# Performance work log

Measured on AMD Instinct MI355X. Metric: run time of the kernel, lower is better.

Reference implementation:

```python
import jax, jax.numpy as jnp
import numpy as np

N = 100000   # nodes
E = 1200000  # edges
IN = 128     # input feature dim
H = 64       # hidden_channels
OUT = 112    # output classes
L = 7        # num_layers
MSG_EPS = 1e-7


def _ln(x, g, b):
    mu = x.mean(-1, keepdims=True)
    v = ((x - mu) ** 2).mean(-1, keepdims=True)
    return (x - mu) / jnp.sqrt(v + 1e-5) * g + b


def _genconv(x, src, dst, t, scale, W1, b1, g1, bb1, W2, b2):
    # message: relu(x_j) + eps  (no edge attrs)
    m = jax.nn.relu(x[src]) + MSG_EPS                     # [E, H]
    z = t * m
    # numerically stable per-dst softmax over incoming edges (per channel)
    zmax = jax.lax.stop_gradient(jax.ops.segment_max(z, dst, num_segments=N))
    e = jnp.exp(z - zmax[dst])
    denom = jax.ops.segment_sum(e, dst, num_segments=N)
    agg = jax.ops.segment_sum(m * e, dst, num_segments=N) / jnp.where(denom > 0, denom, 1.0)
    # MsgNorm: x + scale * ||x|| * normalize(agg)
    msg = agg / jnp.maximum(jnp.linalg.norm(agg, axis=-1, keepdims=True), 1e-12)
    h = x + scale * msg * jnp.linalg.norm(x, axis=-1, keepdims=True)
    # GENConv MLP: Linear(H,2H) -> LayerNorm -> ReLU -> Linear(2H,H)
    u = jax.nn.relu(_ln(h @ W1 + b1, g1, bb1))
    return u @ W2 + b2


def setup_inputs() -> dict:
    key = jax.random.key(0)
    ks = jax.random.split(key, 6)
    s = 0.02
    return dict(
        x=jax.random.normal(ks[0], (N, IN), jnp.float32),
        edge_index=jax.random.randint(ks[1], (2, E), 0, N, dtype=jnp.int32),
        enc_W=jax.random.normal(ks[2], (IN, H), jnp.float32) * s,
        enc_b=jnp.zeros((H,), jnp.float32),
        t=jnp.ones((L,), jnp.float32),
        msg_scale=jnp.ones((L,), jnp.float32),
        W1=jax.random.normal(ks[3], (L, H, 2 * H), jnp.float32) * s,
        b1=jnp.zeros((L, 2 * H), jnp.float32),
        ln1_g=jnp.ones((L, 2 * H), jnp.float32),
        ln1_b=jnp.zeros((L, 2 * H), jnp.float32),
        W2=jax.random.normal(ks[4], (L, 2 * H, H), jnp.float32) * s,
        b2=jnp.zeros((L, H), jnp.float32),
        nrm_g=jnp.ones((L, H), jnp.float32),
        nrm_b=jnp.zeros((L, H), jnp.float32),
        lin_W=jax.random.normal(ks[5], (H, OUT), jnp.float32) * s,
        lin_b=jnp.zeros((OUT,), jnp.float32),
    )


def reference(x, edge_index, enc_W, enc_b, t, msg_scale, W1, b1, ln1_g, ln1_b,
              W2, b2, nrm_g, nrm_b, lin_W, lin_b):
    src, dst = edge_index[0], edge_index[1]
    h = x @ enc_W + enc_b
    # first layer: conv only (DeeperGCN forward applies layers[0].conv directly)
    h = _genconv(h, src, dst, t[0], msg_scale[0], W1[0], b1[0], ln1_g[0], ln1_b[0], W2[0], b2[0])
    # remaining layers: res+ block  x + conv(dropout(relu(norm(x))))  (dropout=identity at eval)
    for i in range(1, L):
        r = jax.nn.relu(_ln(h, nrm_g[i], nrm_b[i]))
        h = h + _genconv(r, src, dst, t[i], msg_scale[i], W1[i], b1[i], ln1_g[i], ln1_b[i], W2[i], b2[i])
    h = jax.nn.relu(_ln(h, nrm_g[0], nrm_b[0]))
    return h @ lin_W + lin_b
```

## Files before the change

### kernel.cpp

```cpp
#include <hip/hip_runtime.h>

#define N_NODES 100000
#define N_EDGES 1200000
#define DIM_IN 128
#define DIM_H 64
#define DIM_H2 128
#define DIM_OUT 112
#define N_LAYERS 7

#define W1P_SZ 4608
#define W2P_SZ 4352
#define WEP_SZ 4352
#define WFP_SZ 4032

typedef __attribute__((ext_vector_type(8))) short bf16x8;
typedef __attribute__((ext_vector_type(4))) float f32x4;

__device__ __forceinline__ float wsum(float v) {
#pragma unroll
  for (int m = 1; m < 64; m <<= 1) v += __shfl_xor(v, m, 64);
  return v;
}

__device__ __forceinline__ unsigned bf16rne(float f) {
  unsigned u = __float_as_uint(f);
  return (u + 0x7fffu + ((u >> 16) & 1u)) >> 16;
}
__device__ __forceinline__ unsigned pack2bf(float lo, float hi) {
  return bf16rne(lo) | (bf16rne(hi) << 16);
}
__device__ __forceinline__ float bflo(unsigned p) { return __uint_as_float(p << 16); }
__device__ __forceinline__ float bfhi(unsigned p) { return __uint_as_float(p & 0xffff0000u); }
__device__ __forceinline__ float bfu(unsigned short u) {
  return __uint_as_float(((unsigned)u) << 16);
}
__device__ __forceinline__ float exp2r(float x) { return __builtin_amdgcn_exp2f(x); }


__global__ void k_zero_i(int* __restrict__ p, int n) {
  int i = blockIdx.x * 256 + threadIdx.x;
  if (i < n) p[i] = 0;
}

__global__ void k_hist(const int* __restrict__ dst, int* __restrict__ counts,
                       int* __restrict__ rank) {
  int e = blockIdx.x * 256 + threadIdx.x;
  if (e < N_EDGES) rank[e] = atomicAdd(&counts[dst[e]], 1);
}

__global__ void k_scan1(const int* __restrict__ counts, int* __restrict__ bsums) {
  __shared__ int sd[256];
  int t = threadIdx.x;
  int i = blockIdx.x * 256 + t;
  sd[t] = (i < N_NODES) ? counts[i] : 0;
  __syncthreads();
  for (int s = 128; s > 0; s >>= 1) {
    if (t < s) sd[t] += sd[t + s];
    __syncthreads();
  }
  if (t == 0) bsums[blockIdx.x] = sd[0];
}

__global__ void k_scan2(int* __restrict__ bsums, int nb) {
  __shared__ int sd[512];
  int t = threadIdx.x;
  int v = (t < nb) ? bsums[t] : 0;
  sd[t] = v;
  __syncthreads();
  for (int o = 1; o < 512; o <<= 1) {
    int add = (t >= o) ? sd[t - o] : 0;
    __syncthreads();
    sd[t] += add;
    __syncthreads();
  }
  if (t < nb) bsums[t] = sd[t] - v;
}

__global__ void k_scan3(const int* __restrict__ counts, const int* __restrict__ bsums,
                        int* __restrict__ offs) {
  __shared__ int sd[256];
  int t = threadIdx.x;
  int i = blockIdx.x * 256 + t;
  int v = (i < N_NODES) ? counts[i] : 0;
  sd[t] = v;
  __syncthreads();
  for (int o = 1; o < 256; o <<= 1) {
    int add = (t >= o) ? sd[t - o] : 0;
    __syncthreads();
    sd[t] += add;
    __syncthreads();
  }
  int excl = sd[t] - v + bsums[blockIdx.x];
  if (i < N_NODES) offs[i] = excl;
  if (i == N_NODES - 1) offs[N_NODES] = excl + v;
}

__global__ void k_scatter(const int* __restrict__ src, const int* __restrict__ dst,
                          const int* __restrict__ rank, const int* __restrict__ offs,
                          int* __restrict__ ssrc) {
  int e = blockIdx.x * 256 + threadIdx.x;
  if (e < N_EDGES) {
    int p = offs[dst[e]] + rank[e];
    ssrc[p] = src[e];
  }
}

__global__ void k_prepack(const float* __restrict__ W1, const float* __restrict__ W2,
                          unsigned* __restrict__ W1p, unsigned* __restrict__ W2p) {
  int L = blockIdx.y;
  const float* w1 = W1 + (size_t)L * DIM_H * DIM_H2;
  const float* w2 = W2 + (size_t)L * DIM_H2 * DIM_H;
  unsigned* o1 = W1p + (size_t)L * W1P_SZ;
  unsigned* o2 = W2p + (size_t)L * W2P_SZ;
  for (int i = blockIdx.x * 256 + threadIdx.x; i < W1P_SZ; i += gridDim.x * 256) {
    int n = i / 36, kp = i - n * 36;
    o1[i] = (kp < 32) ? pack2bf(w1[(size_t)(2 * kp) * DIM_H2 + n],
                                w1[(size_t)(2 * kp + 1) * DIM_H2 + n]) : 0u;
  }
  for (int i = blockIdx.x * 256 + threadIdx.x; i < W2P_SZ; i += gridDim.x * 256) {
    int n = i / 68, kp = i - n * 68;
    o2[i] = (kp < 64) ? pack2bf(w2[(size_t)(2 * kp) * DIM_H + n],
                                w2[(size_t)(2 * kp + 1) * DIM_H + n]) : 0u;
  }
}

__global__ void k_prepack_enc(const float* __restrict__ W, unsigned* __restrict__ Wp) {
  for (int i = blockIdx.x * 256 + threadIdx.x; i < WEP_SZ; i += gridDim.x * 256) {
    int n = i / 68, kp = i - n * 68;
    Wp[i] = (kp < 64) ? pack2bf(W[(size_t)(2 * kp) * DIM_H + n],
                                W[(size_t)(2 * kp + 1) * DIM_H + n]) : 0u;
  }
}

__global__ void k_prepack_fin(const float* __restrict__ W, unsigned* __restrict__ Wp) {
  for (int i = blockIdx.x * 256 + threadIdx.x; i < WFP_SZ; i += gridDim.x * 256) {
    int n = i / 36, kp = i - n * 36;
    Wp[i] = (kp < 32) ? pack2bf(W[(size_t)(2 * kp) * DIM_OUT + n],
                                W[(size_t)(2 * kp + 1) * DIM_OUT + n]) : 0u;
  }
}


__global__ __launch_bounds__(256, 2) void k_encoder(const float* __restrict__ x,
                                                    const unsigned* __restrict__ Wp,
                                                    const float* __restrict__ bias,
                                                    unsigned short* __restrict__ hBf) {
  __shared__ __attribute__((aligned(16))) unsigned sW[WEP_SZ];
  __shared__ __attribute__((aligned(16))) unsigned sxp[32 * 68];
  int t = threadIdx.x;
  int node0 = blockIdx.x * 32;
  int w = t >> 6, lane = t & 63;
  int fr = lane & 15, fq = lane >> 4;
  const uint4* wv4 = (const uint4*)Wp;
  for (int i = t; i < WEP_SZ / 4; i += 256) *(uint4*)&sW[i * 4] = wv4[i];
  for (int i = t; i < 2048; i += 256) {
    int row = i >> 6, kp = i & 63;
    float2 xv = *(const float2*)&x[(size_t)(node0 + row) * DIM_IN + 2 * kp];
    sxp[row * 68 + kp] = pack2bf(xv.x, xv.y);
  }
  __syncthreads();
  f32x4 acc0 = {0.f, 0.f, 0.f, 0.f}, acc1 = acc0;
#pragma unroll
  for (int s = 0; s < 4; s++) {
    int kp0 = s * 16 + fq * 4;
    bf16x8 a0 = *(const bf16x8*)&sxp[fr * 68 + kp0];
    bf16x8 a1 = *(const bf16x8*)&sxp[(16 + fr) * 68 + kp0];
    bf16x8 wf = *(const bf16x8*)&sW[(w * 16 + fr) * 68 + kp0];
    acc0 = __builtin_amdgcn_mfma_f32_16x16x32_bf16(a0, wf, acc0, 0, 0, 0);
    acc1 = __builtin_amdgcn_mfma_f32_16x16x32_bf16(a1, wf, acc1, 0, 0, 0);
  }
  float bv = bias[w * 16 + fr];
#pragma unroll
  for (int r = 0; r < 4; r++) {
    hBf[(size_t)(node0 + fq * 4 + r) * DIM_H + w * 16 + fr] =
        (unsigned short)bf16rne(acc0[r] + bv);
    hBf[(size_t)(node0 + 16 + fq * 4 + r) * DIM_H + w * 16 + fr] =
        (unsigned short)bf16rne(acc1[r] + bv);
  }
}


__global__ __launch_bounds__(256) void k_edge(const unsigned* __restrict__ xin32,
                                              const int* __restrict__ ssrc,
                                              const int* __restrict__ offs,
                                              const float* __restrict__ t_arr,
                                              const float* __restrict__ sc_arr, int layer,
                                              unsigned* __restrict__ hmid32) {
  int t = threadIdx.x;
  int wave = t >> 6, lane = t & 63;
  int half = lane >> 5, cl = lane & 31;
  int v = blockIdx.x * 8 + wave * 2 + half;
  float c2 = t_arr[layer] * 1.4426950408889634f;
  float sc = sc_arr[layer];
  int beg = offs[v], end = offs[v + 1];
  unsigned cl4 = cl << 2;
  const char* xbase = (const char*)xin32;
  unsigned xp = *(const unsigned*)(xbase + (((unsigned)v << 7) + cl4));
  float xv0 = bflo(xp), xv1 = bfhi(xp);
  float D0 = 0.f, S0 = 0.f, D1 = 0.f, S1 = 0.f;
  float D2 = 0.f, S2 = 0.f, D3 = 0.f, S3 = 0.f;
  float D4 = 0.f, S4 = 0.f, D5 = 0.f, S5 = 0.f;
  float D6 = 0.f, S6 = 0.f, D7 = 0.f, S7 = 0.f;
  int e = beg;
  for (; e + 3 < end; e += 4) {
    unsigned o0 = ((unsigned)ssrc[e] << 7) + cl4;
    unsigned o1 = ((unsigned)ssrc[e + 1] << 7) + cl4;
    unsigned o2 = ((unsigned)ssrc[e + 2] << 7) + cl4;
    unsigned o3 = ((unsigned)ssrc[e + 3] << 7) + cl4;
    unsigned u0 = *(const unsigned*)(xbase + o0);
    unsigned u1 = *(const unsigned*)(xbase + o1);
    unsigned u2 = *(const unsigned*)(xbase + o2);
    unsigned u3 = *(const unsigned*)(xbase + o3);
    float a0 = fmaxf(bflo(u0), 0.f), a1 = fmaxf(bfhi(u0), 0.f);
    float b0 = fmaxf(bflo(u1), 0.f), b1 = fmaxf(bfhi(u1), 0.f);
    float g0 = fmaxf(bflo(u2), 0.f), g1 = fmaxf(bfhi(u2), 0.f);
    float h0 = fmaxf(bflo(u3), 0.f), h1 = fmaxf(bfhi(u3), 0.f);
    float ea0 = exp2r(c2 * a0), ea1 = exp2r(c2 * a1);
    float eb0 = exp2r(c2 * b0), eb1 = exp2r(c2 * b1);
    float eg0 = exp2r(c2 * g0), eg1 = exp2r(c2 * g1);
    float eh0 = exp2r(c2 * h0), eh1 = exp2r(c2 * h1);
    D0 += ea0; S0 += a0 * ea0;
    D1 += ea1; S1 += a1 * ea1;
    D2 += eb0; S2 += b0 * eb0;
    D3 += eb1; S3 += b1 * eb1;
    D4 += eg0; S4 += g0 * eg0;
    D5 += eg1; S5 += g1 * eg1;
    D6 += eh0; S6 += h0 * eh0;
    D7 += eh1; S7 += h1 * eh1;
  }
  for (; e < end; ++e) {
    unsigned o0 = ((unsigned)ssrc[e] << 7) + cl4;
    unsigned u0 = *(const unsigned*)(xbase + o0);
    float a0 = fmaxf(bflo(u0), 0.f), a1 = fmaxf(bfhi(u0), 0.f);
    float ea0 = exp2r(c2 * a0), ea1 = exp2r(c2 * a1);
    D0 += ea0; S0 += a0 * ea0;
    D1 += ea1; S1 += a1 * ea1;
  }
  float Da = (D0 + D2) + (D4 + D6), Sa = (S0 + S2) + (S4 + S6);
  float Db = (D1 + D3) + (D5 + D7), Sb = (S1 + S3) + (S5 + S7);
  int has = (end > beg);
  float agg0 = has ? (Sa / Da + 1e-7f) : 0.f;
  float agg1 = has ? (Sb / Db + 1e-7f) : 0.f;
  float na = agg0 * agg0 + agg1 * agg1;
  float nx = xv0 * xv0 + xv1 * xv1;
#pragma unroll
  for (int m = 1; m < 32; m <<= 1) {
    na += __shfl_xor(na, m, 64);
    nx += __shfl_xor(nx, m, 64);
  }
  float inv = sc * sqrtf(nx) / fmaxf(sqrtf(na), 1e-12f);
  float r0 = xv0 + inv * agg0;
  float r1 = xv1 + inv * agg1;
  hmid32[(size_t)v * 32 + cl] = pack2bf(r0, r1);
}


__global__ __launch_bounds__(256, 2) void k_mlp(const unsigned* __restrict__ xin32,
                                                float* __restrict__ h,
                                                unsigned short* __restrict__ rnext,
                                                const unsigned* __restrict__ W1p,
                                                const float* __restrict__ b1,
                                                const float* __restrict__ g1,
                                                const float* __restrict__ bb1,
                                                const unsigned* __restrict__ W2p,
                                                const float* __restrict__ b2,
                                                const float* __restrict__ gn,
                                                const float* __restrict__ bn, int residual) {
  __shared__ unsigned short scr[4][16][136];
  int t = threadIdx.x;
  int w = t >> 6, lane = t & 63;
  int wid = blockIdx.x * 4 + w;
  if (wid >= N_NODES / 16) return;
  int node0 = wid * 16;
  int fr = lane & 15, fq = lane >> 4;

  bf16x8 xa0 = *(const bf16x8*)&xin32[(size_t)(node0 + fr) * 32 + fq * 4];
  bf16x8 xa1 = *(const bf16x8*)&xin32[(size_t)(node0 + fr) * 32 + 16 + fq * 4];
  f32x4 c1[8];
#pragma unroll
  for (int nt = 0; nt < 8; nt++) {
    f32x4 a = {0.f, 0.f, 0.f, 0.f};
    bf16x8 w0 = *(const bf16x8*)&W1p[(size_t)(nt * 16 + fr) * 36 + fq * 4];
    bf16x8 w1 = *(const bf16x8*)&W1p[(size_t)(nt * 16 + fr) * 36 + 16 + fq * 4];
    a = __builtin_amdgcn_mfma_f32_16x16x32_bf16(xa0, w0, a, 0, 0, 0);
    a = __builtin_amdgcn_mfma_f32_16x16x32_bf16(xa1, w1, a, 0, 0, 0);
    c1[nt] = a;
  }
  float b1v[8], g1v[8], bb1v[8];
#pragma unroll
  for (int nt = 0; nt < 8; nt++) {
    b1v[nt] = b1[nt * 16 + fr];
    g1v[nt] = g1[nt * 16 + fr];
    bb1v[nt] = bb1[nt * 16 + fr];
  }
#pragma unroll
  for (int r = 0; r < 4; r++) {
    float s1 = 0.f, s2 = 0.f;
#pragma unroll
    for (int nt = 0; nt < 8; nt++) {
      float u = c1[nt][r] + b1v[nt];
      s1 += u;
      s2 += u * u;
    }
#pragma unroll
    for (int m = 1; m < 16; m <<= 1) {
      s1 += __shfl_xor(s1, m, 64);
      s2 += __shfl_xor(s2, m, 64);
    }
    float mu = s1 * (1.f / 128.f);
    float var = s2 * (1.f / 128.f) - mu * mu;
    float rs = rsqrtf(var + 1e-5f);
    int row = fq * 4 + r;
#pragma unroll
    for (int nt = 0; nt < 8; nt++) {
      float u = c1[nt][r] + b1v[nt];
      u = fmaxf((u - mu) * rs * g1v[nt] + bb1v[nt], 0.f);
      scr[w][row][nt * 16 + fr] = (unsigned short)bf16rne(u);
    }
  }
  bf16x8 ua[4];
#pragma unroll
  for (int s = 0; s < 4; s++) ua[s] = *(const bf16x8*)&scr[w][fr][s * 32 + fq * 8];
  f32x4 c2[4];
#pragma unroll
  for (int nt = 0; nt < 4; nt++) {
    f32x4 a = {0.f, 0.f, 0.f, 0.f};
#pragma unroll
    for (int s = 0; s < 4; s++) {
      bf16x8 wf = *(const bf16x8*)&W2p[(size_t)(nt * 16 + fr) * 68 + s * 16 + fq * 4];
      a = __builtin_amdgcn_mfma_f32_16x16x32_bf16(ua[s], wf, a, 0, 0, 0);
    }
    c2[nt] = a;
  }
  float b2v[4], gv[4], bv[4];
#pragma unroll
  for (int nt = 0; nt < 4; nt++) {
    b2v[nt] = b2[nt * 16 + fr];
    gv[nt] = gn[nt * 16 + fr];
    bv[nt] = bn[nt * 16 + fr];
  }
#pragma unroll
  for (int r = 0; r < 4; r++) {
    int row = fq * 4 + r;
    size_t base = (size_t)(node0 + row) * DIM_H;
    float o0, o1, o2, o3, s1, s2;
    o0 = c2[0][r] + b2v[0];
    o1 = c2[1][r] + b2v[1];
    o2 = c2[2][r] + b2v[2];
    o3 = c2[3][r] + b2v[3];
    if (residual) {
      o0 += h[base + 0 * 16 + fr];
      o1 += h[base + 1 * 16 + fr];
      o2 += h[base + 2 * 16 + fr];
      o3 += h[base + 3 * 16 + fr];
    }
    s1 = (o0 + o1) + (o2 + o3);
    s2 = (o0 * o0 + o1 * o1) + (o2 * o2 + o3 * o3);
#pragma unroll
    for (int m = 1; m < 16; m <<= 1) {
      s1 += __shfl_xor(s1, m, 64);
      s2 += __shfl_xor(s2, m, 64);
    }
    float mu = s1 * (1.f / 64.f);
    float var = s2 * (1.f / 64.f) - mu * mu;
    float rs = rsqrtf(var + 1e-5f);
    h[base + 0 * 16 + fr] = o0;
    h[base + 1 * 16 + fr] = o1;
    h[base + 2 * 16 + fr] = o2;
    h[base + 3 * 16 + fr] = o3;
    rnext[base + 0 * 16 + fr] = (unsigned short)bf16rne(fmaxf((o0 - mu) * rs * gv[0] + bv[0], 0.f));
    rnext[base + 1 * 16 + fr] = (unsigned short)bf16rne(fmaxf((o1 - mu) * rs * gv[1] + bv[1], 0.f));
    rnext[base + 2 * 16 + fr] = (unsigned short)bf16rne(fmaxf((o2 - mu) * rs * gv[2] + bv[2], 0.f));
    rnext[base + 3 * 16 + fr] = (unsigned short)bf16rne(fmaxf((o3 - mu) * rs * gv[3] + bv[3], 0.f));
  }
}


__global__ __launch_bounds__(256, 2) void k_final(const unsigned* __restrict__ rB32,
                                                  const unsigned* __restrict__ Wp,
                                                  const float* __restrict__ bias,
                                                  float* __restrict__ out) {
  int t = threadIdx.x;
  int w = t >> 6, lane = t & 63;
  int wid = blockIdx.x * 4 + w;
  if (wid >= N_NODES / 16) return;
  int node0 = wid * 16;
  int fr = lane & 15, fq = lane >> 4;
  bf16x8 xa0 = *(const bf16x8*)&rB32[(size_t)(node0 + fr) * 32 + fq * 4];
  bf16x8 xa1 = *(const bf16x8*)&rB32[(size_t)(node0 + fr) * 32 + 16 + fq * 4];
#pragma unroll
  for (int nt = 0; nt < 7; nt++) {
    f32x4 a = {0.f, 0.f, 0.f, 0.f};
    bf16x8 w0 = *(const bf16x8*)&Wp[(size_t)(nt * 16 + fr) * 36 + fq * 4];
    bf16x8 w1 = *(const bf16x8*)&Wp[(size_t)(nt * 16 + fr) * 36 + 16 + fq * 4];
    a = __builtin_amdgcn_mfma_f32_16x16x32_bf16(xa0, w0, a, 0, 0, 0);
    a = __builtin_amdgcn_mfma_f32_16x16x32_bf16(xa1, w1, a, 0, 0, 0);
    float bv = bias[nt * 16 + fr];
#pragma unroll
    for (int r = 0; r < 4; r++)
      out[(size_t)(node0 + fq * 4 + r) * DIM_OUT + nt * 16 + fr] = a[r] + bv;
  }
}


extern "C" void kernel_launch(void* const* d_in, const int* in_sizes, int n_in,
                              void* d_out, int out_size, void* d_ws, size_t ws_size,
                              hipStream_t stream) {
  const float* x = (const float*)d_in[0];
  const int* ei = (const int*)d_in[1];
  const float* encW = (const float*)d_in[2];
  const float* encb = (const float*)d_in[3];
  const float* t_arr = (const float*)d_in[4];
  const float* sc_arr = (const float*)d_in[5];
  const float* W1 = (const float*)d_in[6];
  const float* b1 = (const float*)d_in[7];
  const float* g1 = (const float*)d_in[8];
  const float* bb1 = (const float*)d_in[9];
  const float* W2 = (const float*)d_in[10];
  const float* b2 = (const float*)d_in[11];
  const float* ng = (const float*)d_in[12];
  const float* nbias = (const float*)d_in[13];
  const float* linW = (const float*)d_in[14];
  const float* linb = (const float*)d_in[15];

  float* hA = (float*)d_ws;
  unsigned short* mCbf = (unsigned short*)(hA + (size_t)N_NODES * DIM_H);
  unsigned short* rBf = mCbf + (size_t)N_NODES * DIM_H;
  unsigned short* hBf = rBf + (size_t)N_NODES * DIM_H;
  int* ssrc = (int*)(hBf + (size_t)N_NODES * DIM_H);
  int* rank = ssrc + N_EDGES;
  int* offs = rank + N_EDGES;
  int* counts = offs + (N_NODES + 1);
  int* bsums = counts + N_NODES;
  unsigned* W1p = (unsigned*)(((uintptr_t)(bsums + 512) + 15) & ~(uintptr_t)15);
  unsigned* W2p = W1p + (size_t)N_LAYERS * W1P_SZ;
  unsigned* Wep = W2p + (size_t)N_LAYERS * W2P_SZ;
  unsigned* Wfp = Wep + WEP_SZ;

  const int* srcI = ei;
  const int* dstI = ei + N_EDGES;

  const int nbScan = (N_NODES + 255) / 256;
  const int nbEdge = (N_EDGES + 255) / 256;
  const int nbWave = (N_NODES / 16 + 3) / 4;

  k_zero_i<<<nbScan, 256, 0, stream>>>(counts, N_NODES);
  k_hist<<<nbEdge, 256, 0, stream>>>(dstI, counts, rank);
  k_prepack<<<dim3(3, N_LAYERS), 256, 0, stream>>>(W1, W2, W1p, W2p);
  k_prepack_enc<<<3, 256, 0, stream>>>(encW, Wep);
  k_prepack_fin<<<3, 256, 0, stream>>>(linW, Wfp);
  k_scan1<<<nbScan, 256, 0, stream>>>(counts, bsums);
  k_scan2<<<1, 512, 0, stream>>>(bsums, nbScan);
  k_scan3<<<nbScan, 256, 0, stream>>>(counts, bsums, offs);
  k_scatter<<<nbEdge, 256, 0, stream>>>(srcI, dstI, rank, offs, ssrc);

  k_encoder<<<N_NODES / 32, 256, 0, stream>>>(x, Wep, encb, hBf);

  for (int i = 0; i < N_LAYERS; i++) {
    int nx = (i + 1 < N_LAYERS) ? (i + 1) : 0;
    const unsigned* gin32 = (const unsigned*)((i == 0) ? hBf : rBf);
    k_edge<<<N_NODES / 8, 256, 0, stream>>>(gin32, ssrc, offs, t_arr, sc_arr, i,
                                            (unsigned*)mCbf);
    k_mlp<<<nbWave, 256, 0, stream>>>(
        (const unsigned*)mCbf, hA, rBf, W1p + (size_t)i * W1P_SZ, b1 + i * DIM_H2,
        g1 + i * DIM_H2, bb1 + i * DIM_H2, W2p + (size_t)i * W2P_SZ, b2 + i * DIM_H,
        ng + nx * DIM_H, nbias + nx * DIM_H, (i > 0) ? 1 : 0);
  }

  k_final<<<nbWave, 256, 0, stream>>>((const unsigned*)rBf, Wfp, linb, (float*)d_out);
}
```

Measured before the change: 585.6 us.

## Partition histogram atomics, unroll edge gather by 8, skip ReLU after first layer

The degree histogram now uses 8 partitioned count arrays, chosen by block index, to cut atomic contention on hot destination counters. The scan kernels sum the partitions and write per-partition prefix offsets, which the scatter uses to place edges. The edge aggregation kernel unrolls the gather loop to 8 edges so more loads are in flight. It is also templated to drop the ReLU for layers after the first, whose inputs are already ReLU outputs. The costs are an 8x larger count array to zero and scan, and higher register pressure in the edge kernel.

Result: faster. 555.8 us (-5.1%).

```diff
diff --git a/kernel.cpp b/kernel.cpp
--- a/kernel.cpp
+++ b/kernel.cpp
@@ -42,17 +42,23 @@
   if (i < n) p[i] = 0;
 }
 
-__global__ void k_hist(const int* __restrict__ dst, int* __restrict__ counts,
+__global__ void k_hist(const int* __restrict__ dst, int* __restrict__ counts8,
                        int* __restrict__ rank) {
   int e = blockIdx.x * 256 + threadIdx.x;
-  if (e < N_EDGES) rank[e] = atomicAdd(&counts[dst[e]], 1);
-}
-
-__global__ void k_scan1(const int* __restrict__ counts, int* __restrict__ bsums) {
+  int p = blockIdx.x & 7;
+  if (e < N_EDGES) rank[e] = atomicAdd(&counts8[(size_t)p * N_NODES + dst[e]], 1);
+}
+
+__global__ void k_scan1(const int* __restrict__ counts8, int* __restrict__ bsums) {
   __shared__ int sd[256];
   int t = threadIdx.x;
   int i = blockIdx.x * 256 + t;
-  sd[t] = (i < N_NODES) ? counts[i] : 0;
+  int v = 0;
+  if (i < N_NODES) {
+#pragma unroll
+    for (int p = 0; p < 8; p++) v += counts8[(size_t)p * N_NODES + i];
+  }
+  sd[t] = v;
   __syncthreads();
   for (int s = 128; s > 0; s >>= 1) {
     if (t < s) sd[t] += sd[t + s];
@@ -76,12 +82,20 @@
   if (t < nb) bsums[t] = sd[t] - v;
 }
 
-__global__ void k_scan3(const int* __restrict__ counts, const int* __restrict__ bsums,
+__global__ void k_scan3(int* __restrict__ counts8, const int* __restrict__ bsums,
                         int* __restrict__ offs) {
   __shared__ int sd[256];
   int t = threadIdx.x;
   int i = blockIdx.x * 256 + t;
-  int v = (i < N_NODES) ? counts[i] : 0;
+  int c[8];
+  int v = 0;
+  if (i < N_NODES) {
+#pragma unroll
+    for (int p = 0; p < 8; p++) {
+      c[p] = counts8[(size_t)p * N_NODES + i];
+      v += c[p];
+    }
+  }
   sd[t] = v;
   __syncthreads();
   for (int o = 1; o < 256; o <<= 1) {
@@ -91,16 +105,26 @@
     __syncthreads();
   }
   int excl = sd[t] - v + bsums[blockIdx.x];
-  if (i < N_NODES) offs[i] = excl;
+  if (i < N_NODES) {
+    offs[i] = excl;
+    int run = 0;
+#pragma unroll
+    for (int p = 0; p < 8; p++) {
+      counts8[(size_t)p * N_NODES + i] = run;
+      run += c[p];
+    }
+  }
   if (i == N_NODES - 1) offs[N_NODES] = excl + v;
 }
 
 __global__ void k_scatter(const int* __restrict__ src, const int* __restrict__ dst,
                           const int* __restrict__ rank, const int* __restrict__ offs,
-                          int* __restrict__ ssrc) {
+                          const int* __restrict__ soff8, int* __restrict__ ssrc) {
   int e = blockIdx.x * 256 + threadIdx.x;
   if (e < N_EDGES) {
-    int p = offs[dst[e]] + rank[e];
+    int d = dst[e];
+    int part = (e >> 8) & 7;
+    int p = offs[d] + soff8[(size_t)part * N_NODES + d] + rank[e];
     ssrc[p] = src[e];
   }
 }
@@ -180,6 +204,7 @@
 }
 
 
+template <int RELU>
 __global__ __launch_bounds__(256) void k_edge(const unsigned* __restrict__ xin32,
                                               const int* __restrict__ ssrc,
                                               const int* __restrict__ offs,
@@ -202,7 +227,54 @@
   float D4 = 0.f, S4 = 0.f, D5 = 0.f, S5 = 0.f;
   float D6 = 0.f, S6 = 0.f, D7 = 0.f, S7 = 0.f;
   int e = beg;
-  for (; e + 3 < end; e += 4) {
+#define CH(u, lo, hi)                                   \
+  float lo = RELU ? fmaxf(bflo(u), 0.f) : bflo(u);      \
+  float hi = RELU ? fmaxf(bfhi(u), 0.f) : bfhi(u);
+  for (; e + 7 < end; e += 8) {
+    unsigned o0 = ((unsigned)ssrc[e] << 7) + cl4;
+    unsigned o1 = ((unsigned)ssrc[e + 1] << 7) + cl4;
+    unsigned o2 = ((unsigned)ssrc[e + 2] << 7) + cl4;
+    unsigned o3 = ((unsigned)ssrc[e + 3] << 7) + cl4;
+    unsigned o4 = ((unsigned)ssrc[e + 4] << 7) + cl4;
+    unsigned o5 = ((unsigned)ssrc[e + 5] << 7) + cl4;
+    unsigned o6 = ((unsigned)ssrc[e + 6] << 7) + cl4;
+    unsigned o7 = ((unsigned)ssrc[e + 7] << 7) + cl4;
+    unsigned u0 = *(const unsigned*)(xbase + o0);
+    unsigned u1 = *(const unsigned*)(xbase + o1);
+    unsigned u2 = *(const unsigned*)(xbase + o2);
+    unsigned u3 = *(const unsigned*)(xbase + o3);
+    unsigned u4 = *(const unsigned*)(xbase + o4);
+    unsigned u5 = *(const unsigned*)(xbase + o5);
+    unsigned u6 = *(const unsigned*)(xbase + o6);
+    unsigned u7 = *(const unsigned*)(xbase + o7);
+    CH(u0, a0, a1) CH(u1, b0, b1) CH(u2, g0, g1) CH(u3, h0, h1)
+    CH(u4, i0, i1) CH(u5, j0, j1) CH(u6, k0, k1) CH(u7, l0, l1)
+    float ea0 = exp2r(c2 * a0), ea1 = exp2r(c2 * a1);
+    float eb0 = exp2r(c2 * b0), eb1 = exp2r(c2 * b1);
+    float eg0 = exp2r(c2 * g0), eg1 = exp2r(c2 * g1);
+    float eh0 = exp2r(c2 * h0), eh1 = exp2r(c2 * h1);
+    float ei0 = exp2r(c2 * i0), ei1 = exp2r(c2 * i1);
+    float ej0 = exp2r(c2 * j0), ej1 = exp2r(c2 * j1);
+    float ek0 = exp2r(c2 * k0), ek1 = exp2r(c2 * k1);
+    float el0 = exp2r(c2 * l0), el1 = exp2r(c2 * l1);
+    D0 += ea0; S0 += a0 * ea0;
+    D1 += ea1; S1 += a1 * ea1;
+    D2 += eb0; S2 += b0 * eb0;
+    D3 += eb1; S3 += b1 * eb1;
+    D4 += eg0; S4 += g0 * eg0;
+    D5 += eg1; S5 += g1 * eg1;
+    D6 += eh0; S6 += h0 * eh0;
+    D7 += eh1; S7 += h1 * eh1;
+    D0 += ei0; S0 += i0 * ei0;
+    D1 += ei1; S1 += i1 * ei1;
+    D2 += ej0; S2 += j0 * ej0;
+    D3 += ej1; S3 += j1 * ej1;
+    D4 += ek0; S4 += k0 * ek0;
+    D5 += ek1; S5 += k1 * ek1;
+    D6 += el0; S6 += l0 * el0;
+    D7 += el1; S7 += l1 * el1;
+  }
+  if (e + 3 < end) {
     unsigned o0 = ((unsigned)ssrc[e] << 7) + cl4;
     unsigned o1 = ((unsigned)ssrc[e + 1] << 7) + cl4;
     unsigned o2 = ((unsigned)ssrc[e + 2] << 7) + cl4;
@@ -211,10 +283,7 @@
     unsigned u1 = *(const unsigned*)(xbase + o1);
     unsigned u2 = *(const unsigned*)(xbase + o2);
     unsigned u3 = *(const unsigned*)(xbase + o3);
-    float a0 = fmaxf(bflo(u0), 0.f), a1 = fmaxf(bfhi(u0), 0.f);
-    float b0 = fmaxf(bflo(u1), 0.f), b1 = fmaxf(bfhi(u1), 0.f);
-    float g0 = fmaxf(bflo(u2), 0.f), g1 = fmaxf(bfhi(u2), 0.f);
-    float h0 = fmaxf(bflo(u3), 0.f), h1 = fmaxf(bfhi(u3), 0.f);
+    CH(u0, a0, a1) CH(u1, b0, b1) CH(u2, g0, g1) CH(u3, h0, h1)
     float ea0 = exp2r(c2 * a0), ea1 = exp2r(c2 * a1);
     float eb0 = exp2r(c2 * b0), eb1 = exp2r(c2 * b1);
     float eg0 = exp2r(c2 * g0), eg1 = exp2r(c2 * g1);
@@ -227,15 +296,17 @@
     D5 += eg1; S5 += g1 * eg1;
     D6 += eh0; S6 += h0 * eh0;
     D7 += eh1; S7 += h1 * eh1;
+    e += 4;
   }
   for (; e < end; ++e) {
     unsigned o0 = ((unsigned)ssrc[e] << 7) + cl4;
     unsigned u0 = *(const unsigned*)(xbase + o0);
-    float a0 = fmaxf(bflo(u0), 0.f), a1 = fmaxf(bfhi(u0), 0.f);
+    CH(u0, a0, a1)
     float ea0 = exp2r(c2 * a0), ea1 = exp2r(c2 * a1);
     D0 += ea0; S0 += a0 * ea0;
     D1 += ea1; S1 += a1 * ea1;
   }
+#undef CH
   float Da = (D0 + D2) + (D4 + D6), Sa = (S0 + S2) + (S4 + S6);
   float Db = (D1 + D3) + (D5 + D7), Sb = (S1 + S3) + (S5 + S7);
   int has = (end > beg);
@@ -430,8 +501,8 @@
   int* ssrc = (int*)(hBf + (size_t)N_NODES * DIM_H);
   int* rank = ssrc + N_EDGES;
   int* offs = rank + N_EDGES;
-  int* counts = offs + (N_NODES + 1);
-  int* bsums = counts + N_NODES;
+  int* counts8 = offs + (N_NODES + 1);
+  int* bsums = counts8 + 8 * N_NODES;
   unsigned* W1p = (unsigned*)(((uintptr_t)(bsums + 512) + 15) & ~(uintptr_t)15);
   unsigned* W2p = W1p + (size_t)N_LAYERS * W1P_SZ;
   unsigned* Wep = W2p + (size_t)N_LAYERS * W2P_SZ;
@@ -444,23 +515,27 @@
   const int nbEdge = (N_EDGES + 255) / 256;
   const int nbWave = (N_NODES / 16 + 3) / 4;
 
-  k_zero_i<<<nbScan, 256, 0, stream>>>(counts, N_NODES);
-  k_hist<<<nbEdge, 256, 0, stream>>>(dstI, counts, rank);
+  k_zero_i<<<(8 * N_NODES + 255) / 256, 256, 0, stream>>>(counts8, 8 * N_NODES);
+  k_hist<<<nbEdge, 256, 0, stream>>>(dstI, counts8, rank);
   k_prepack<<<dim3(3, N_LAYERS), 256, 0, stream>>>(W1, W2, W1p, W2p);
   k_prepack_enc<<<3, 256, 0, stream>>>(encW, Wep);
   k_prepack_fin<<<3, 256, 0, stream>>>(linW, Wfp);
-  k_scan1<<<nbScan, 256, 0, stream>>>(counts, bsums);
+  k_scan1<<<nbScan, 256, 0, stream>>>(counts8, bsums);
   k_scan2<<<1, 512, 0, stream>>>(bsums, nbScan);
-  k_scan3<<<nbScan, 256, 0, stream>>>(counts, bsums, offs);
-  k_scatter<<<nbEdge, 256, 0, stream>>>(srcI, dstI, rank, offs, ssrc);
+  k_scan3<<<nbScan, 256, 0, stream>>>(counts8, bsums, offs);
+  k_scatter<<<nbEdge, 256, 0, stream>>>(srcI, dstI, rank, offs, counts8, ssrc);
 
   k_encoder<<<N_NODES / 32, 256, 0, stream>>>(x, Wep, encb, hBf);
 
   for (int i = 0; i < N_LAYERS; i++) {
     int nx = (i + 1 < N_LAYERS) ? (i + 1) : 0;
     const unsigned* gin32 = (const unsigned*)((i == 0) ? hBf : rBf);
-    k_edge<<<N_NODES / 8, 256, 0, stream>>>(gin32, ssrc, offs, t_arr, sc_arr, i,
-                                            (unsigned*)mCbf);
+    if (i == 0)
+      k_edge<1><<<N_NODES / 8, 256, 0, stream>>>(gin32, ssrc, offs, t_arr, sc_arr, i,
+                                                 (unsigned*)mCbf);
+    else
+      k_edge<0><<<N_NODES / 8, 256, 0, stream>>>(gin32, ssrc, offs, t_arr, sc_arr, i,
+                                                 (unsigned*)mCbf);
     k_mlp<<<nbWave, 256, 0, stream>>>(
         (const unsigned*)mCbf, hA, rBf, W1p + (size_t)i * W1P_SZ, b1 + i * DIM_H2,
         g1 + i * DIM_H2, bb1 + i * DIM_H2, W2p + (size_t)i * W2P_SZ, b2 + i * DIM_H,
```

## Fuse edge aggregation into per-layer MLP kernel with ping-pong activation buffers

Applied to the files above, without the earlier changes.

Merges the softmax edge-aggregation kernel into the MLP kernel. Each wave aggregates its 16 nodes and writes the bf16 result into shared memory instead of a global mid buffer, so one launch and one global write/read pass per layer go away. It also unrolls the gather loop to 8 edges, skips the ReLU for layers past the first (inputs are already post-ReLU), and ping-pongs the r buffers because the gather reads neighbours the same kernel would otherwise overwrite. The risk is lower occupancy and less latency hiding for the gather: there are far fewer waves (one per 16 nodes), and launch_bounds(256,2) forces more registers.

Result: slower. 688.5 us (+17.6%).

```diff
diff --git a/kernel.cpp b/kernel.cpp
--- a/kernel.cpp
+++ b/kernel.cpp
@@ -16,12 +16,6 @@
 typedef __attribute__((ext_vector_type(8))) short bf16x8;
 typedef __attribute__((ext_vector_type(4))) float f32x4;
 
-__device__ __forceinline__ float wsum(float v) {
-#pragma unroll
-  for (int m = 1; m < 64; m <<= 1) v += __shfl_xor(v, m, 64);
-  return v;
-}
-
 __device__ __forceinline__ unsigned bf16rne(float f) {
   unsigned u = __float_as_uint(f);
   return (u + 0x7fffu + ((u >> 16) & 1u)) >> 16;
@@ -31,9 +25,6 @@
 }
 __device__ __forceinline__ float bflo(unsigned p) { return __uint_as_float(p << 16); }
 __device__ __forceinline__ float bfhi(unsigned p) { return __uint_as_float(p & 0xffff0000u); }
-__device__ __forceinline__ float bfu(unsigned short u) {
-  return __uint_as_float(((unsigned)u) << 16);
-}
 __device__ __forceinline__ float exp2r(float x) { return __builtin_amdgcn_exp2f(x); }
 
 
@@ -104,6 +95,7 @@
     ssrc[p] = src[e];
   }
 }
+
 
 __global__ void k_prepack(const float* __restrict__ W1, const float* __restrict__ W2,
                           unsigned* __restrict__ W1p, unsigned* __restrict__ W2p) {
@@ -180,92 +172,25 @@
 }
 
 
-__global__ __launch_bounds__(256) void k_edge(const unsigned* __restrict__ xin32,
-                                              const int* __restrict__ ssrc,
-                                              const int* __restrict__ offs,
-                                              const float* __restrict__ t_arr,
-                                              const float* __restrict__ sc_arr, int layer,
-                                              unsigned* __restrict__ hmid32) {
-  int t = threadIdx.x;
-  int wave = t >> 6, lane = t & 63;
-  int half = lane >> 5, cl = lane & 31;
-  int v = blockIdx.x * 8 + wave * 2 + half;
-  float c2 = t_arr[layer] * 1.4426950408889634f;
-  float sc = sc_arr[layer];
-  int beg = offs[v], end = offs[v + 1];
-  unsigned cl4 = cl << 2;
-  const char* xbase = (const char*)xin32;
-  unsigned xp = *(const unsigned*)(xbase + (((unsigned)v << 7) + cl4));
-  float xv0 = bflo(xp), xv1 = bfhi(xp);
-  float D0 = 0.f, S0 = 0.f, D1 = 0.f, S1 = 0.f;
-  float D2 = 0.f, S2 = 0.f, D3 = 0.f, S3 = 0.f;
-  float D4 = 0.f, S4 = 0.f, D5 = 0.f, S5 = 0.f;
-  float D6 = 0.f, S6 = 0.f, D7 = 0.f, S7 = 0.f;
-  int e = beg;
-  for (; e + 3 < end; e += 4) {
-    unsigned o0 = ((unsigned)ssrc[e] << 7) + cl4;
-    unsigned o1 = ((unsigned)ssrc[e + 1] << 7) + cl4;
-    unsigned o2 = ((unsigned)ssrc[e + 2] << 7) + cl4;
-    unsigned o3 = ((unsigned)ssrc[e + 3] << 7) + cl4;
-    unsigned u0 = *(const unsigned*)(xbase + o0);
-    unsigned u1 = *(const unsigned*)(xbase + o1);
-    unsigned u2 = *(const unsigned*)(xbase + o2);
-    unsigned u3 = *(const unsigned*)(xbase + o3);
-    float a0 = fmaxf(bflo(u0), 0.f), a1 = fmaxf(bfhi(u0), 0.f);
-    float b0 = fmaxf(bflo(u1), 0.f), b1 = fmaxf(bfhi(u1), 0.f);
-    float g0 = fmaxf(bflo(u2), 0.f), g1 = fmaxf(bfhi(u2), 0.f);
-    float h0 = fmaxf(bflo(u3), 0.f), h1 = fmaxf(bfhi(u3), 0.f);
-    float ea0 = exp2r(c2 * a0), ea1 = exp2r(c2 * a1);
-    float eb0 = exp2r(c2 * b0), eb1 = exp2r(c2 * b1);
-    float eg0 = exp2r(c2 * g0), eg1 = exp2r(c2 * g1);
-    float eh0 = exp2r(c2 * h0), eh1 = exp2r(c2 * h1);
-    D0 += ea0; S0 += a0 * ea0;
-    D1 += ea1; S1 += a1 * ea1;
-    D2 += eb0; S2 += b0 * eb0;
-    D3 += eb1; S3 += b1 * eb1;
-    D4 += eg0; S4 += g0 * eg0;
-    D5 += eg1; S5 += g1 * eg1;
-    D6 += eh0; S6 += h0 * eh0;
-    D7 += eh1; S7 += h1 * eh1;
-  }
-  for (; e < end; ++e) {
-    unsigned o0 = ((unsigned)ssrc[e] << 7) + cl4;
-    unsigned u0 = *(const unsigned*)(xbase + o0);
-    float a0 = fmaxf(bflo(u0), 0.f), a1 = fmaxf(bfhi(u0), 0.f);
-    float ea0 = exp2r(c2 * a0), ea1 = exp2r(c2 * a1);
-    D0 += ea0; S0 += a0 * ea0;
-    D1 += ea1; S1 += a1 * ea1;
-  }
-  float Da = (D0 + D2) + (D4 + D6), Sa = (S0 + S2) + (S4 + S6);
-  float Db = (D1 + D3) + (D5 + D7), Sb = (S1 + S3) + (S5 + S7);
-  int has = (end > beg);
-  float agg0 = has ? (Sa / Da + 1e-7f) : 0.f;
-  float agg1 = has ? (Sb / Db + 1e-7f) : 0.f;
-  float na = agg0 * agg0 + agg1 * agg1;
-  float nx = xv0 * xv0 + xv1 * xv1;
-#pragma unroll
-  for (int m = 1; m < 32; m <<= 1) {
-    na += __shfl_xor(na, m, 64);
-    nx += __shfl_xor(nx, m, 64);
-  }
-  float inv = sc * sqrtf(nx) / fmaxf(sqrtf(na), 1e-12f);
-  float r0 = xv0 + inv * agg0;
-  float r1 = xv1 + inv * agg1;
-  hmid32[(size_t)v * 32 + cl] = pack2bf(r0, r1);
-}
-
-
-__global__ __launch_bounds__(256, 2) void k_mlp(const unsigned* __restrict__ xin32,
-                                                float* __restrict__ h,
-                                                unsigned short* __restrict__ rnext,
-                                                const unsigned* __restrict__ W1p,
-                                                const float* __restrict__ b1,
-                                                const float* __restrict__ g1,
-                                                const float* __restrict__ bb1,
-                                                const unsigned* __restrict__ W2p,
-                                                const float* __restrict__ b2,
-                                                const float* __restrict__ gn,
-                                                const float* __restrict__ bn, int residual) {
+template <int RELU>
+__global__ __launch_bounds__(256, 2) void k_layer(const unsigned* __restrict__ xin32,
+                                                  const int* __restrict__ ssrc,
+                                                  const int* __restrict__ offs,
+                                                  const float* __restrict__ t_arr,
+                                                  const float* __restrict__ sc_arr,
+                                                  int layer,
+                                                  float* __restrict__ h,
+                                                  unsigned short* __restrict__ rnext,
+                                                  const unsigned* __restrict__ W1p,
+                                                  const float* __restrict__ b1,
+                                                  const float* __restrict__ g1,
+                                                  const float* __restrict__ bb1,
+                                                  const unsigned* __restrict__ W2p,
+                                                  const float* __restrict__ b2,
+                                                  const float* __restrict__ gn,
+                                                  const float* __restrict__ bn,
+                                                  int residual) {
+  __shared__ unsigned sxw[4][16 * 36];
   __shared__ unsigned short scr[4][16][136];
   int t = threadIdx.x;
   int w = t >> 6, lane = t & 63;
@@ -273,9 +198,123 @@
   if (wid >= N_NODES / 16) return;
   int node0 = wid * 16;
   int fr = lane & 15, fq = lane >> 4;
-
-  bf16x8 xa0 = *(const bf16x8*)&xin32[(size_t)(node0 + fr) * 32 + fq * 4];
-  bf16x8 xa1 = *(const bf16x8*)&xin32[(size_t)(node0 + fr) * 32 + 16 + fq * 4];
+  int half = lane >> 5, cl = lane & 31;
+
+  {
+    float c2 = t_arr[layer] * 1.4426950408889634f;
+    float sc = sc_arr[layer];
+    unsigned cl4 = cl << 2;
+    const char* xbase = (const char*)xin32;
+#pragma unroll 1
+    for (int p = 0; p < 8; p++) {
+      int v = node0 + 2 * p + half;
+      int beg = offs[v], end = offs[v + 1];
+      unsigned xp = *(const unsigned*)(xbase + (((unsigned)v << 7) + cl4));
+      float xv0 = bflo(xp), xv1 = bfhi(xp);
+      float D0 = 0.f, S0 = 0.f, D1 = 0.f, S1 = 0.f;
+      float D2 = 0.f, S2 = 0.f, D3 = 0.f, S3 = 0.f;
+      float D4 = 0.f, S4 = 0.f, D5 = 0.f, S5 = 0.f;
+      float D6 = 0.f, S6 = 0.f, D7 = 0.f, S7 = 0.f;
+      int e = beg;
+#define CH(u, lo, hi)                              \
+  float lo = RELU ? fmaxf(bflo(u), 0.f) : bflo(u); \
+  float hi = RELU ? fmaxf(bfhi(u), 0.f) : bfhi(u);
+      for (; e + 7 < end; e += 8) {
+        unsigned o0 = ((unsigned)ssrc[e] << 7) + cl4;
+        unsigned o1 = ((unsigned)ssrc[e + 1] << 7) + cl4;
+        unsigned o2 = ((unsigned)ssrc[e + 2] << 7) + cl4;
+        unsigned o3 = ((unsigned)ssrc[e + 3] << 7) + cl4;
+        unsigned o4 = ((unsigned)ssrc[e + 4] << 7) + cl4;
+        unsigned o5 = ((unsigned)ssrc[e + 5] << 7) + cl4;
+        unsigned o6 = ((unsigned)ssrc[e + 6] << 7) + cl4;
+        unsigned o7 = ((unsigned)ssrc[e + 7] << 7) + cl4;
+        unsigned u0 = *(const unsigned*)(xbase + o0);
+        unsigned u1 = *(const unsigned*)(xbase + o1);
+        unsigned u2 = *(const unsigned*)(xbase + o2);
+        unsigned u3 = *(const unsigned*)(xbase + o3);
+        unsigned u4 = *(const unsigned*)(xbase + o4);
+        unsigned u5 = *(const unsigned*)(xbase + o5);
+        unsigned u6 = *(const unsigned*)(xbase + o6);
+        unsigned u7 = *(const unsigned*)(xbase + o7);
+        CH(u0, a0, a1) CH(u1, b0, b1) CH(u2, g0, g1) CH(u3, h0, h1)
+        CH(u4, i0, i1) CH(u5, j0, j1) CH(u6, k0, k1) CH(u7, l0, l1)
+        float ea0 = exp2r(c2 * a0), ea1 = exp2r(c2 * a1);
+        float eb0 = exp2r(c2 * b0), eb1 = exp2r(c2 * b1);
+        float eg0 = exp2r(c2 * g0), eg1 = exp2r(c2 * g1);
+        float eh0 = exp2r(c2 * h0), eh1 = exp2r(c2 * h1);
+        float ei0 = exp2r(c2 * i0), ei1 = exp2r(c2 * i1);
+        float ej0 = exp2r(c2 * j0), ej1 = exp2r(c2 * j1);
+        float ek0 = exp2r(c2 * k0), ek1 = exp2r(c2 * k1);
+        float el0 = exp2r(c2 * l0), el1 = exp2r(c2 * l1);
+        D0 += ea0; S0 += a0 * ea0;
+        D1 += ea1; S1 += a1 * ea1;
+        D2 += eb0; S2 += b0 * eb0;
+        D3 += eb1; S3 += b1 * eb1;
+        D4 += eg0; S4 += g0 * eg0;
+        D5 += eg1; S5 += g1 * eg1;
+        D6 += eh0; S6 += h0 * eh0;
+        D7 += eh1; S7 += h1 * eh1;
+        D0 += ei0; S0 += i0 * ei0;
+        D1 += ei1; S1 += i1 * ei1;
+        D2 += ej0; S2 += j0 * ej0;
+        D3 += ej1; S3 += j1 * ej1;
+        D4 += ek0; S4 += k0 * ek0;
+        D5 += ek1; S5 += k1 * ek1;
+        D6 += el0; S6 += l0 * el0;
+        D7 += el1; S7 += l1 * el1;
+      }
+      if (e + 3 < end) {
+        unsigned o0 = ((unsigned)ssrc[e] << 7) + cl4;
+        unsigned o1 = ((unsigned)ssrc[e + 1] << 7) + cl4;
+        unsigned o2 = ((unsigned)ssrc[e + 2] << 7) + cl4;
+        unsigned o3 = ((unsigned)ssrc[e + 3] << 7) + cl4;
+        unsigned u0 = *(const unsigned*)(xbase + o0);
+        unsigned u1 = *(const unsigned*)(xbase + o1);
+        unsigned u2 = *(const unsigned*)(xbase + o2);
+        unsigned u3 = *(const unsigned*)(xbase + o3);
+        CH(u0, a0, a1) CH(u1, b0, b1) CH(u2, g0, g1) CH(u3, h0, h1)
+        float ea0 = exp2r(c2 * a0), ea1 = exp2r(c2 * a1);
+        float eb0 = exp2r(c2 * b0), eb1 = exp2r(c2 * b1);
+        float eg0 = exp2r(c2 * g0), eg1 = exp2r(c2 * g1);
+        float eh0 = exp2r(c2 * h0), eh1 = exp2r(c2 * h1);
+        D0 += ea0; S0 += a0 * ea0;
+        D1 += ea1; S1 += a1 * ea1;
+        D2 += eb0; S2 += b0 * eb0;
+        D3 += eb1; S3 += b1 * eb1;
+        D4 += eg0; S4 += g0 * eg0;
+        D5 += eg1; S5 += g1 * eg1;
+        D6 += eh0; S6 += h0 * eh0;
+        D7 += eh1; S7 += h1 * eh1;
+        e += 4;
+      }
+      for (; e < end; ++e) {
+        unsigned o0 = ((unsigned)ssrc[e] << 7) + cl4;
+        unsigned u0 = *(const unsigned*)(xbase + o0);
+        CH(u0, a0, a1)
+        float ea0 = exp2r(c2 * a0), ea1 = exp2r(c2 * a1);
+        D0 += ea0; S0 += a0 * ea0;
+        D1 += ea1; S1 += a1 * ea1;
+      }
+#undef CH
+      float Da = (D0 + D2) + (D4 + D6), Sa = (S0 + S2) + (S4 + S6);
+      float Db = (D1 + D3) + (D5 + D7), Sb = (S1 + S3) + (S5 + S7);
+      int has = (end > beg);
+      float agg0 = has ? (Sa / Da + 1e-7f) : 0.f;
+      float agg1 = has ? (Sb / Db + 1e-7f) : 0.f;
+      float na = agg0 * agg0 + agg1 * agg1;
+      float nx = xv0 * xv0 + xv1 * xv1;
+#pragma unroll
+      for (int m = 1; m < 32; m <<= 1) {
+        na += __shfl_xor(na, m, 64);
+        nx += __shfl_xor(nx, m, 64);
+      }
+      float inv = sc * sqrtf(nx) / fmaxf(sqrtf(na), 1e-12f);
+      sxw[w][(2 * p + half) * 36 + cl] = pack2bf(xv0 + inv * agg0, xv1 + inv * agg1);
+    }
+  }
+
+  bf16x8 xa0 = *(const bf16x8*)&sxw[w][fr * 36 + fq * 4];
+  bf16x8 xa1 = *(const bf16x8*)&sxw[w][fr * 36 + 16 + fq * 4];
   f32x4 c1[8];
 #pragma unroll
   for (int nt = 0; nt < 8; nt++) {
@@ -424,9 +463,9 @@
   const float* linb = (const float*)d_in[15];
 
   float* hA = (float*)d_ws;
-  unsigned short* mCbf = (unsigned short*)(hA + (size_t)N_NODES * DIM_H);
-  unsigned short* rBf = mCbf + (size_t)N_NODES * DIM_H;
-  unsigned short* hBf = rBf + (size_t)N_NODES * DIM_H;
+  unsigned short* rA = (unsigned short*)(hA + (size_t)N_NODES * DIM_H);
+  unsigned short* rB = rA + (size_t)N_NODES * DIM_H;
+  unsigned short* hBf = rB + (size_t)N_NODES * DIM_H;
   int* ssrc = (int*)(hBf + (size_t)N_NODES * DIM_H);
   int* rank = ssrc + N_EDGES;
   int* offs = rank + N_EDGES;
@@ -458,14 +497,19 @@
 
   for (int i = 0; i < N_LAYERS; i++) {
     int nx = (i + 1 < N_LAYERS) ? (i + 1) : 0;
-    const unsigned* gin32 = (const unsigned*)((i == 0) ? hBf : rBf);
-    k_edge<<<N_NODES / 8, 256, 0, stream>>>(gin32, ssrc, offs, t_arr, sc_arr, i,
-                                            (unsigned*)mCbf);
-    k_mlp<<<nbWave, 256, 0, stream>>>(
-        (const unsigned*)mCbf, hA, rBf, W1p + (size_t)i * W1P_SZ, b1 + i * DIM_H2,
-        g1 + i * DIM_H2, bb1 + i * DIM_H2, W2p + (size_t)i * W2P_SZ, b2 + i * DIM_H,
-        ng + nx * DIM_H, nbias + nx * DIM_H, (i > 0) ? 1 : 0);
-  }
-
-  k_final<<<nbWave, 256, 0, stream>>>((const unsigned*)rBf, Wfp, linb, (float*)d_out);
-}
+    const unsigned* rin = (const unsigned*)((i == 0) ? hBf : ((i & 1) ? rA : rB));
+    unsigned short* rout = (i & 1) ? rB : rA;
+    if (i == 0)
+      k_layer<1><<<nbWave, 256, 0, stream>>>(
+          rin, ssrc, offs, t_arr, sc_arr, i, hA, rout, W1p + (size_t)i * W1P_SZ,
+          b1 + i * DIM_H2, g1 + i * DIM_H2, bb1 + i * DIM_H2, W2p + (size_t)i * W2P_SZ,
+          b2 + i * DIM_H, ng + nx * DIM_H, nbias + nx * DIM_H, 0);
+    else
+      k_layer<0><<<nbWave, 256, 0, stream>>>(
+          rin, ssrc, offs, t_arr, sc_arr, i, hA, rout, W1p + (size_t)i * W1P_SZ,
+          b1 + i * DIM_H2, g1 + i * DIM_H2, bb1 + i * DIM_H2, W2p + (size_t)i * W2P_SZ,
+          b2 + i * DIM_H, ng + nx * DIM_H, nbias + nx * DIM_H, 1);
+  }
+
+  k_final<<<nbWave, 256, 0, stream>>>((const unsigned*)rA, Wfp, linb, (float*)d_out);
+}
```
